# Optimization experiments

Measured on AMD Instinct MI355X. Metric: run time of the kernel, lower is better.

## Reference

```python
import jax, jax.numpy as jnp
import numpy as np

NUM_HEADS = 16
HEAD_SIZE = 64
D_MODEL = NUM_HEADS * HEAD_SIZE  # 1024


def setup_inputs() -> dict:
    key = jax.random.key(0)
    k_in, k_ctx, k_q, k_k, k_v, k_o, k_b = jax.random.split(key, 7)
    B, Sq, Skv, D = 4, 2048, 2048, D_MODEL
    inputs = jax.random.normal(k_in, (B, Sq, D), dtype=jnp.float32)
    context = jax.random.normal(k_ctx, (B, Skv, D), dtype=jnp.float32)
    s = 0.02
    Wq = jax.random.normal(k_q, (D, D), dtype=jnp.float32) * s
    Wk = jax.random.normal(k_k, (D, D), dtype=jnp.float32) * s
    Wv = jax.random.normal(k_v, (D, D), dtype=jnp.float32) * s
    Wo = jax.random.normal(k_o, (D, D), dtype=jnp.float32) * s
    bo = jnp.zeros((D,), dtype=jnp.float32)
    return {"inputs": inputs, "context": context, "Wq": Wq, "Wk": Wk,
            "Wv": Wv, "Wo": Wo, "bo": bo}


def reference(inputs, context, Wq, Wk, Wv, Wo, bo):
    # inputs: [B, Sq, D]; context: [B, Skv, D]
    B, Sq, _ = inputs.shape
    H, Dh = NUM_HEADS, HEAD_SIZE
    scale = Dh ** -0.5
    q = (inputs @ Wq).reshape(B, Sq, H, Dh)          # [B,Sq,H,Dh]
    k = (context @ Wk).reshape(B, -1, H, Dh)          # [B,Skv,H,Dh]
    v = (context @ Wv).reshape(B, -1, H, Dh)
    # The chunked online-softmax recurrence in the source is exactly softmax attention.
    scores = jnp.einsum('bqhd,bkhd->bhqk', q, k) * scale
    probs = jax.nn.softmax(scores, axis=-1)
    attn = jnp.einsum('bhqk,bkhd->bqhd', probs, v)    # [B,Sq,H,Dh]
    out = attn.reshape(B, Sq, H * Dh)
    return out @ Wo + bo
```

## Files before the change

### kernel.cpp

```cpp
#include <hip/hip_runtime.h>
#include <hip/hip_bf16.h>


#define D_MODEL 1024
#define NHEAD   16
#define DHEAD   64
#define BATCH   4
#define SEQ     2048
#define MROWS   (BATCH * SEQ)
#define WP      ((size_t)D_MODEL * D_MODEL)

typedef unsigned short u16;
typedef __attribute__((ext_vector_type(8))) _Float16       f16x8;
typedef __attribute__((ext_vector_type(2))) _Float16       f16x2;
typedef __attribute__((ext_vector_type(4))) float          f32x4;
typedef __attribute__((ext_vector_type(8))) unsigned short u16x8;
typedef __attribute__((ext_vector_type(4))) unsigned short u16x4;

__device__ __forceinline__ u16 f2h(float x) {
    union { _Float16 h; u16 u; } cv;
    cv.h = (_Float16)x;
    return cv.u;
}

__device__ __forceinline__ unsigned pkrtz(float a, float b) {
    unsigned r;
    asm("v_cvt_pkrtz_f16_f32 %0, %1, %2" : "=v"(r) : "v"(a), "v"(b));
    return r;
}

__device__ __forceinline__ f32x4 mfma16h(f16x8 a, f16x8 b, f32x4 c) {
    return __builtin_amdgcn_mfma_f32_16x16x32_f16(a, b, c, 0, 0, 0);
}

__device__ __forceinline__ float exp2fast(float x) {
    float r;
    asm("v_exp_f32 %0, %1" : "=v"(r) : "v"(x));
    return r;
}

__device__ __forceinline__ void glds16(const void* g, void* l) {
    __builtin_amdgcn_global_load_lds(
        (const __attribute__((address_space(1))) void*)g,
        (__attribute__((address_space(3))) void*)l, 16, 0, 0);
}

__global__ __launch_bounds__(256) void prep(const float* __restrict__ ctx,
                                            const float* __restrict__ inp,
                                            u16* __restrict__ ctx16,
                                            u16* __restrict__ in16,
                                            const float* __restrict__ W0,
                                            const float* __restrict__ W1,
                                            const float* __restrict__ W2,
                                            const float* __restrict__ W3,
                                            u16* __restrict__ wt, float qscale) {
    __shared__ u16 th[64 * 64];
    const int id = blockIdx.x;
    const int t = threadIdx.x;

    if (id < 4096) {
        const size_t i = ((size_t)id * 256 + t) * 8;
        {
            float4 v0 = *(const float4*)(ctx + i);
            float4 v1 = *(const float4*)(ctx + i + 4);
            u16x8 h;
            h[0] = f2h(v0.x); h[1] = f2h(v0.y); h[2] = f2h(v0.z); h[3] = f2h(v0.w);
            h[4] = f2h(v1.x); h[5] = f2h(v1.y); h[6] = f2h(v1.z); h[7] = f2h(v1.w);
            *(u16x8*)(ctx16 + i) = h;
        }
        {
            float4 v0 = *(const float4*)(inp + i);
            float4 v1 = *(const float4*)(inp + i + 4);
            u16x8 h;
            h[0] = f2h(v0.x); h[1] = f2h(v0.y); h[2] = f2h(v0.z); h[3] = f2h(v0.w);
            h[4] = f2h(v1.x); h[5] = f2h(v1.y); h[6] = f2h(v1.z); h[7] = f2h(v1.w);
            *(u16x8*)(in16 + i) = h;
        }
        return;
    }

    const int id2 = id - 4096;
    const int z = id2 >> 8;
    const int rem = id2 & 255;
    const float* W = (z == 0) ? W0 : (z == 1) ? W1 : (z == 2) ? W2 : W3;
    const float scale = (z == 2) ? qscale : 1.0f;
    u16* T = wt + (size_t)z * WP;
    const int k0 = (rem & 15) * 64, n0 = (rem >> 4) * 64;

#pragma unroll
    for (int rep = 0; rep < 4; ++rep) {
        int kr = (t >> 4) + 16 * rep;
        int nc = (t & 15) * 4;
        float4 v = *(const float4*)(W + (size_t)(k0 + kr) * D_MODEL + n0 + nc);
#pragma unroll
        for (int u = 0; u < 4; ++u) {
            int n = nc + u;
            th[n * 64 + (kr ^ (8 * ((n >> 3) & 7)))] = f2h(((const float*)&v)[u] * scale);
        }
    }
    __syncthreads();
#pragma unroll
    for (int rep = 0; rep < 2; ++rep) {
        int n = (t >> 3) + 32 * rep;
        int kb = (t & 7) * 8;
        int a = n * 64 + (kb ^ (8 * ((n >> 3) & 7)));
        *(u16x8*)(T + (size_t)(n0 + n) * D_MODEL + k0 + kb) = *(const u16x8*)&th[a];
    }
}

__global__ __launch_bounds__(256) void gemm_proj(const u16* __restrict__ Actx,
                                                 const u16* __restrict__ Ainp,
                                                 const u16* __restrict__ Bh,
                                                 u16* __restrict__ Kf,
                                                 u16* __restrict__ Vimg,
                                                 u16* __restrict__ Qf) {
    const int K = 1024;
    __shared__ u16 sA[128 * 32];
    __shared__ u16 sB[128 * 32];

    const int t = threadIdx.x;
    const int w = t >> 6, l = t & 63, g = l >> 4, lr = l & 15;
    const int wrow = (w >> 1) * 64, wcol = (w & 1) * 64;

    const int bid = blockIdx.x;
    const int vg = bid >> 9;
    const int inner = bid & 511;
    const int wgs = (inner & 7) * 64 + (inner >> 3);
    const int bm = wgs >> 3, bn8 = wgs & 7;
    const int bn = vg * 8 + bn8;

    const u16* A16 = (vg < 2) ? Actx : Ainp;

    f32x4 acc[4][4];
#pragma unroll
    for (int i = 0; i < 4; ++i)
#pragma unroll
        for (int j = 0; j < 4; ++j) acc[i][j] = (f32x4){0.f, 0.f, 0.f, 0.f};

    const int srow = t >> 2;
    const int scg  = (((t & 3) ^ ((srow >> 1) & 3)) * 8);
    const int lofs0 = t * 8;
    const int gsw  = (g ^ ((lr >> 1) & 3)) * 8;

    for (int k0 = 0; k0 < K; k0 += 32) {
#pragma unroll
        for (int rep = 0; rep < 2; ++rep) {
            const int row  = srow + 64 * rep;
            const int lofs = lofs0 + rep * 2048;
            glds16(A16 + (size_t)(bm * 128 + row) * K + k0 + scg, &sA[lofs]);
            glds16(Bh  + (size_t)(bn * 128 + row) * K + k0 + scg, &sB[lofs]);
        }
        __syncthreads();

        f16x8 a[4], b[4];
#pragma unroll
        for (int f = 0; f < 4; ++f) {
            a[f] = *(const f16x8*)&sA[(wrow + f * 16 + lr) * 32 + gsw];
            b[f] = *(const f16x8*)&sB[(wcol + f * 16 + lr) * 32 + gsw];
        }
        __builtin_amdgcn_s_setprio(1);
#pragma unroll
        for (int fi = 0; fi < 4; ++fi)
#pragma unroll
            for (int fj = 0; fj < 4; ++fj)
                acc[fi][fj] = mfma16h(a[fi], b[fj], acc[fi][fj]);
        __builtin_amdgcn_s_setprio(0);
        __syncthreads();
    }

    if (vg == 0) {
#pragma unroll
        for (int fj = 0; fj < 4; ++fj) {
            const int colg = bn8 * 128 + wcol + fj * 16 + lr;
#pragma unroll
            for (int fi = 0; fi < 4; ++fi) {
                const int rowb = bm * 128 + wrow + fi * 16 + 4 * g;
#pragma unroll
                for (int j = 0; j < 4; ++j)
                    Kf[(size_t)(rowb + j) * D_MODEL + colg] = f2h(acc[fi][fj][j]);
            }
        }
    } else if (vg == 1) {
        const int rowb0 = bm * 128 + wrow;
        const int bidx = rowb0 >> 11;
        const int tile = (rowb0 & 2047) >> 6;
#pragma unroll
        for (int fj = 0; fj < 4; ++fj) {
            const int vcol = bn8 * 128 + wcol + fj * 16 + lr;
            const int vh = vcol >> 6, vd = vcol & 63;
            const size_t tbase = ((size_t)((bidx * NHEAD + vh) * 32) + tile) * 4096;
            const int dsw = vd & 7;
#pragma unroll
            for (int fi = 0; fi < 4; ++fi) {
                const int qp = g | ((fi >> 1) << 2);
                const int i0 = (fi & 1) << 2;
                const int q  = qp ^ dsw;
                u16x4 hv;
#pragma unroll
                for (int j = 0; j < 4; ++j) hv[j] = f2h(acc[fi][fj][j]);
                *(u16x4*)(Vimg + tbase + vd * 64 + 8 * q + i0) = hv;
            }
        }
    } else {
#pragma unroll
        for (int fj = 0; fj < 4; ++fj) {
            const int colg = bn8 * 128 + wcol + fj * 16 + lr;
#pragma unroll
            for (int fi = 0; fi < 4; ++fi) {
                const int rowb = bm * 128 + wrow + fi * 16 + 4 * g;
#pragma unroll
                for (int j = 0; j < 4; ++j)
                    Qf[(size_t)(rowb + j) * D_MODEL + colg] = f2h(acc[fi][fj][j]);
            }
        }
    }
}

__global__ __launch_bounds__(256) void gemm_out(const u16* __restrict__ A16,
                                                const u16* __restrict__ Bh,
                                                const float* __restrict__ bias,
                                                float* __restrict__ Cf) {
    const int K = 1024, N = 1024;
    __shared__ u16 sA[64 * 32];
    __shared__ u16 sB[128 * 32];

    const int t = threadIdx.x;
    const int w = t >> 6, l = t & 63, g = l >> 4, lr = l & 15;
    const int wrow = (w >> 1) * 32, wcol = (w & 1) * 64;

    const int bid = blockIdx.x;
    const int wg = (bid & 7) * 128 + (bid >> 3);
    const int bm = wg & 127, bn = wg >> 7;

    f32x4 acc[2][4];
#pragma unroll
    for (int i = 0; i < 2; ++i)
#pragma unroll
        for (int j = 0; j < 4; ++j) acc[i][j] = (f32x4){0.f, 0.f, 0.f, 0.f};

    const int srow = t >> 2;
    const int scg  = (((t & 3) ^ ((srow >> 1) & 3)) * 8);
    const int lofs0 = t * 8;
    const int gsw  = (g ^ ((lr >> 1) & 3)) * 8;

    for (int k0 = 0; k0 < K; k0 += 32) {
        glds16(A16 + (size_t)(bm * 64 + srow) * K + k0 + scg, &sA[lofs0]);
#pragma unroll
        for (int rep = 0; rep < 2; ++rep) {
            const int row = srow + 64 * rep;
            glds16(Bh + (size_t)(bn * 128 + row) * K + k0 + scg, &sB[lofs0 + rep * 2048]);
        }
        __syncthreads();

        f16x8 a[2], b[4];
#pragma unroll
        for (int f = 0; f < 2; ++f)
            a[f] = *(const f16x8*)&sA[(wrow + f * 16 + lr) * 32 + gsw];
#pragma unroll
        for (int f = 0; f < 4; ++f)
            b[f] = *(const f16x8*)&sB[(wcol + f * 16 + lr) * 32 + gsw];
        __builtin_amdgcn_s_setprio(1);
#pragma unroll
        for (int fi = 0; fi < 2; ++fi)
#pragma unroll
            for (int fj = 0; fj < 4; ++fj)
                acc[fi][fj] = mfma16h(a[fi], b[fj], acc[fi][fj]);
        __builtin_amdgcn_s_setprio(0);
        __syncthreads();
    }

#pragma unroll
    for (int fj = 0; fj < 4; ++fj) {
        const int colg = bn * 128 + wcol + fj * 16 + lr;
        const float bv = bias[colg];
#pragma unroll
        for (int fi = 0; fi < 2; ++fi) {
            const int rowb = bm * 64 + wrow + fi * 16 + 4 * g;
#pragma unroll
            for (int j = 0; j < 4; ++j)
                Cf[(size_t)(rowb + j) * N + colg] = acc[fi][fj][j] + bv;
        }
    }
}

__global__ __launch_bounds__(512) void attn_mfma8(const u16* __restrict__ Qf,
                                                  const u16* __restrict__ Kf,
                                                  const u16* __restrict__ Vimg,
                                                  u16* __restrict__ Af16) {
    const int bid  = blockIdx.x;
    const int wgid = (bid & 7) * 64 + (bid >> 3);
    const int qt = wgid & 7;
    const int hb = wgid >> 3;
    const int h = hb & 15, b = hb >> 4;

    const int t = threadIdx.x, w = t >> 6, l = t & 63, g = l >> 4, lr = l & 15;

    __shared__ u16 Ks[2][4096];
    __shared__ u16 Vs[2][4096];

    f16x8 qf[2][2];
#pragma unroll
    for (int qg = 0; qg < 2; ++qg) {
        const size_t qb = (size_t)(b * SEQ + qt * 256 + w * 32 + qg * 16 + lr) * D_MODEL + h * DHEAD;
#pragma unroll
        for (int c = 0; c < 2; ++c)
            qf[qg][c] = *(const f16x8*)(Qf + qb + 32 * c + 8 * g);
    }

    f32x4 o[2][4];
#pragma unroll
    for (int qg = 0; qg < 2; ++qg)
#pragma unroll
        for (int c = 0; c < 4; ++c) o[qg][c] = (f32x4){0.f, 0.f, 0.f, 0.f};
    float lsum[2] = {0.f, 0.f};

    const u16* Kh = Kf + (size_t)(b * SEQ) * D_MODEL + h * DHEAD;
    const size_t vtb = (size_t)((b * NHEAD + h) * 32) * 4096;

    const int kr_ = t >> 3, kd0 = (t & 7) * 8;
    const int ksrc  = kd0 ^ ((kr_ & 7) << 3);
    const int klofs = t * 8;
    const int kkey  = (lr & 7) << 3;

    const f16x2 ones2 = {(_Float16)1.0f, (_Float16)1.0f};

    auto stage = [&](int bb, int kv0) {
        glds16(Kh + (size_t)(kv0 + kr_) * D_MODEL + ksrc, &Ks[bb][klofs]);
        glds16(Vimg + vtb + (size_t)(kv0 >> 6) * 4096 + (size_t)t * 8, &Vs[bb][klofs]);
    };

    stage(0, 0);

    for (int it = 0; it < SEQ / 64; ++it) {
        const int cb = it & 1;
        __syncthreads();
        if (it < SEQ / 64 - 1) stage(cb ^ 1, (it + 1) << 6);

        f32x4 s[2][4];
#pragma unroll
        for (int qg = 0; qg < 2; ++qg)
#pragma unroll
            for (int rt = 0; rt < 4; ++rt) s[qg][rt] = (f32x4){-4.f, -4.f, -4.f, -4.f};
        __builtin_amdgcn_s_setprio(1);
#pragma unroll
        for (int rt = 0; rt < 4; ++rt) {
            const int rb = (16 * rt + lr) * 64;
#pragma unroll
            for (int c = 0; c < 2; ++c) {
                const int p = rb + ((8 * g + 32 * c) ^ kkey);
                f16x8 k8 = *(const f16x8*)&Ks[cb][p];
#pragma unroll
                for (int qg = 0; qg < 2; ++qg)
                    s[qg][rt] = mfma16h(k8, qf[qg][c], s[qg][rt]);
            }
        }
        __builtin_amdgcn_s_setprio(0);

#pragma unroll
        for (int qg = 0; qg < 2; ++qg) {
#pragma unroll
            for (int rt = 0; rt < 4; ++rt)
#pragma unroll
                for (int j = 0; j < 4; ++j)
                    s[qg][rt][j] = exp2fast(s[qg][rt][j]);

            float rs = 0.f;
            f16x8 pbq[2];
#pragma unroll
            for (int ks = 0; ks < 2; ++ks) {
                union { unsigned w_[4]; f16x8 v; } pk;
#pragma unroll
                for (int pr = 0; pr < 4; ++pr) {
                    const int rt = 2 * ks + (pr >> 1);
                    const int j0 = (pr & 1) * 2;
                    const unsigned pw = pkrtz(s[qg][rt][j0], s[qg][rt][j0 + 1]);
                    pk.w_[pr] = pw;
                    union { unsigned w_; f16x2 h2; } cv;
                    cv.w_ = pw;
                    rs = __builtin_amdgcn_fdot2(cv.h2, ones2, rs, false);
                }
                pbq[ks] = pk.v;
            }
            lsum[qg] += rs;

            __builtin_amdgcn_s_setprio(1);
#pragma unroll
            for (int ks = 0; ks < 2; ++ks)
#pragma unroll
                for (int c = 0; c < 4; ++c) {
                    const int dv = 16 * c + lr;
                    f16x8 v8 = *(const f16x8*)&Vs[cb][dv * 64 + ((8 * g + 32 * ks) ^ ((dv & 7) << 3))];
                    o[qg][c] = mfma16h(v8, pbq[ks], o[qg][c]);
                }
            __builtin_amdgcn_s_setprio(0);
        }
    }

#pragma unroll
    for (int qg = 0; qg < 2; ++qg) {
        lsum[qg] += __shfl_xor(lsum[qg], 16);
        lsum[qg] += __shfl_xor(lsum[qg], 32);
        const float inv = 1.f / lsum[qg];
        u16* op = Af16 + (size_t)(b * SEQ + qt * 256 + w * 32 + qg * 16 + lr) * D_MODEL + h * DHEAD;
#pragma unroll
        for (int c = 0; c < 4; ++c) {
            u16x4 hv;
#pragma unroll
            for (int j = 0; j < 4; ++j) hv[j] = f2h(o[qg][c][j] * inv);
            *(u16x4*)(op + 16 * c + 4 * g) = hv;
        }
    }
}

extern "C" void kernel_launch(void* const* d_in, const int* in_sizes, int n_in,
                              void* d_out, int out_size, void* d_ws, size_t ws_size,
                              hipStream_t stream) {
    const float* inputs  = (const float*)d_in[0];
    const float* context = (const float*)d_in[1];
    const float* Wq      = (const float*)d_in[2];
    const float* Wk      = (const float*)d_in[3];
    const float* Wv      = (const float*)d_in[4];
    const float* Wo      = (const float*)d_in[5];
    const float* bo      = (const float*)d_in[6];
    float* out = (float*)d_out;

    const size_t P = (size_t)MROWS * D_MODEL;

    u16* base  = (u16*)d_ws;
    u16* ctx16 = base;
    u16* in16  = base + P;
    u16* kf    = base + 2 * P;
    u16* vimg  = base + 3 * P;
    u16* qf    = base + 4 * P;
    u16* af    = base + 5 * P;
    u16* wt    = base + 6 * P;
    u16* woh   = wt + 3 * WP;

    const float QSCALE = 0.18033688011112042f;

    prep<<<dim3(5120), dim3(256), 0, stream>>>(context, inputs, ctx16, in16,
                                               Wk, Wv, Wq, Wo, wt, QSCALE);

    gemm_proj<<<dim3(1536), dim3(256), 0, stream>>>(ctx16, in16, wt, kf, vimg, qf);

    attn_mfma8<<<dim3(512), dim3(512), 0, stream>>>(qf, kf, vimg, af);

    gemm_out<<<dim3(1024), dim3(256), 0, stream>>>(af, woh, bo, out);
}
```

Measured before the change: 223.2 us.

## Double-buffer LDS tiles in projection and output GEMMs

```diff
diff --git a/kernel.cpp b/kernel.cpp
--- a/kernel.cpp
+++ b/kernel.cpp
@@ -115,8 +115,8 @@
                                                  u16* __restrict__ Vimg,
                                                  u16* __restrict__ Qf) {
     const int K = 1024;
-    __shared__ u16 sA[128 * 32];
-    __shared__ u16 sB[128 * 32];
+    __shared__ u16 sA[2][128 * 32];
+    __shared__ u16 sB[2][128 * 32];
 
     const int t = threadIdx.x;
     const int w = t >> 6, l = t & 63, g = l >> 4, lr = l & 15;
@@ -142,21 +142,30 @@
     const int lofs0 = t * 8;
     const int gsw  = (g ^ ((lr >> 1) & 3)) * 8;
 
+    const u16* Abase = A16 + (size_t)(bm * 128) * K + scg;
+    const u16* Bbase = Bh  + (size_t)(bn * 128) * K + scg;
+
+    auto stage = [&](int buf, int k0) {
+#pragma unroll
+        for (int rep = 0; rep < 2; ++rep) {
+            const size_t go = (size_t)(srow + 64 * rep) * K + k0;
+            glds16(Abase + go, &sA[buf][lofs0 + rep * 2048]);
+            glds16(Bbase + go, &sB[buf][lofs0 + rep * 2048]);
+        }
+    };
+
+    stage(0, 0);
+
     for (int k0 = 0; k0 < K; k0 += 32) {
-#pragma unroll
-        for (int rep = 0; rep < 2; ++rep) {
-            const int row  = srow + 64 * rep;
-            const int lofs = lofs0 + rep * 2048;
-            glds16(A16 + (size_t)(bm * 128 + row) * K + k0 + scg, &sA[lofs]);
-            glds16(Bh  + (size_t)(bn * 128 + row) * K + k0 + scg, &sB[lofs]);
-        }
+        const int cb = (k0 >> 5) & 1;
         __syncthreads();
+        if (k0 + 32 < K) stage(cb ^ 1, k0 + 32);
 
         f16x8 a[4], b[4];
 #pragma unroll
         for (int f = 0; f < 4; ++f) {
-            a[f] = *(const f16x8*)&sA[(wrow + f * 16 + lr) * 32 + gsw];
-            b[f] = *(const f16x8*)&sB[(wcol + f * 16 + lr) * 32 + gsw];
+            a[f] = *(const f16x8*)&sA[cb][(wrow + f * 16 + lr) * 32 + gsw];
+            b[f] = *(const f16x8*)&sB[cb][(wcol + f * 16 + lr) * 32 + gsw];
         }
         __builtin_amdgcn_s_setprio(1);
 #pragma unroll
@@ -165,7 +174,6 @@
             for (int fj = 0; fj < 4; ++fj)
                 acc[fi][fj] = mfma16h(a[fi], b[fj], acc[fi][fj]);
         __builtin_amdgcn_s_setprio(0);
-        __syncthreads();
     }
 
     if (vg == 0) {
@@ -221,8 +229,8 @@
                                                 const float* __restrict__ bias,
                                                 float* __restrict__ Cf) {
     const int K = 1024, N = 1024;
-    __shared__ u16 sA[64 * 32];
-    __shared__ u16 sB[128 * 32];
+    __shared__ u16 sA[2][64 * 32];
+    __shared__ u16 sB[2][128 * 32];
 
     const int t = threadIdx.x;
     const int w = t >> 6, l = t & 63, g = l >> 4, lr = l & 15;
@@ -243,22 +251,30 @@
     const int lofs0 = t * 8;
     const int gsw  = (g ^ ((lr >> 1) & 3)) * 8;
 
+    const u16* Abase = A16 + (size_t)(bm * 64) * K + scg;
+    const u16* Bbase = Bh  + (size_t)(bn * 128) * K + scg;
+
+    auto stage = [&](int buf, int k0) {
+        glds16(Abase + (size_t)srow * K + k0, &sA[buf][lofs0]);
+#pragma unroll
+        for (int rep = 0; rep < 2; ++rep)
+            glds16(Bbase + (size_t)(srow + 64 * rep) * K + k0, &sB[buf][lofs0 + rep * 2048]);
+    };
+
+    stage(0, 0);
+
     for (int k0 = 0; k0 < K; k0 += 32) {
-        glds16(A16 + (size_t)(bm * 64 + srow) * K + k0 + scg, &sA[lofs0]);
-#pragma unroll
-        for (int rep = 0; rep < 2; ++rep) {
-            const int row = srow + 64 * rep;
-            glds16(Bh + (size_t)(bn * 128 + row) * K + k0 + scg, &sB[lofs0 + rep * 2048]);
-        }
+        const int cb = (k0 >> 5) & 1;
         __syncthreads();
+        if (k0 + 32 < K) stage(cb ^ 1, k0 + 32);
 
         f16x8 a[2], b[4];
 #pragma unroll
         for (int f = 0; f < 2; ++f)
-            a[f] = *(const f16x8*)&sA[(wrow + f * 16 + lr) * 32 + gsw];
+            a[f] = *(const f16x8*)&sA[cb][(wrow + f * 16 + lr) * 32 + gsw];
 #pragma unroll
         for (int f = 0; f < 4; ++f)
-            b[f] = *(const f16x8*)&sB[(wcol + f * 16 + lr) * 32 + gsw];
+            b[f] = *(const f16x8*)&sB[cb][(wcol + f * 16 + lr) * 32 + gsw];
         __builtin_amdgcn_s_setprio(1);
 #pragma unroll
         for (int fi = 0; fi < 2; ++fi)
@@ -266,7 +282,6 @@
             for (int fj = 0; fj < 4; ++fj)
                 acc[fi][fj] = mfma16h(a[fi], b[fj], acc[fi][fj]);
         __builtin_amdgcn_s_setprio(0);
-        __syncthreads();
     }
 
 #pragma unroll
```

New measurement: 206.4 us, median of 2. 7.5% less time.
